# Kernel optimization log

Measured on AMD Instinct MI355X. Metric: run time of the kernel, lower is better.

## Reference

```python
import jax, jax.numpy as jnp
import numpy as np

N_CLASS = 20
N_SIGMA = 2
H = W = 512
B = 4
N_INST = 32
W_INST, W_VAR, W_SEED = 1.0, 10.0, 1.0
FG_WEIGHT = 10.0


def _xym():
    # channel 0: x along width, channel 1: y along height (matches torch buffer)
    xm = jnp.broadcast_to(jnp.linspace(0.0, 1.0, W)[None, :], (H, W))
    ym = jnp.broadcast_to(jnp.linspace(0.0, 1.0, H)[:, None], (H, W))
    return jnp.stack([xm, ym], axis=0)  # [2, H, W]


def lovasz_hinge_flat(logits, gt, valid):
    # logits, gt (0/1 float), valid (bool), all flat [P]; ignored pixels excluded
    P = logits.shape[0]
    vf = valid.astype(logits.dtype)
    signs = 2.0 * gt - 1.0
    # push ignored pixels to the end of the descending sort; relu(-1e9)=0 kills them
    errors = jnp.where(valid, 1.0 - logits * signs, -1e9)
    errors_sorted, perm = jax.lax.top_k(errors, P)  # descending
    gt_sorted = jnp.take(gt * vf, perm)
    v_sorted = jnp.take(vf, perm)
    gts = jnp.sum(gt * vf)
    inter = gts - jnp.cumsum(gt_sorted)
    union = gts + jnp.cumsum((1.0 - gt_sorted) * v_sorted)
    jac = 1.0 - inter / jnp.maximum(union, 1e-9)
    jac = jnp.concatenate([jac[:1], jac[1:] - jac[:-1]])
    return jnp.sum(jax.nn.relu(errors_sorted) * jac)


def _per_image(pred_b, inst_b, lab_b, xym, fg_w, n_inst):
    spatial_emb = jnp.tanh(pred_b[:2]) + xym            # [2,H,W]
    sigma = pred_b[2:2 + N_SIGMA]                       # [n_sigma,H,W]
    seed = jax.nn.sigmoid(pred_b[2 + N_SIGMA:2 + N_SIGMA + N_CLASS])  # [C,H,W]
    inst = inst_b[0]
    lab = lab_b[0]
    valid = (lab != 255)

    # background seed loss: sum over classes of seed^2 on pixels not of that class
    cls_ids = jnp.arange(N_CLASS)
    bg = (lab[None] != (cls_ids + 1)[:, None, None]) & valid[None]
    seed_bg = jnp.sum(jnp.square(seed) * bg)

    def per_inst(iid):
        m = (inst == iid)
        mf = m.astype(pred_b.dtype)
        cnt = jnp.maximum(jnp.sum(mf), 1.0)
        # to_center=True: center is mean coordinate of instance pixels
        center = jnp.sum(xym * mf[None], axis=(1, 2)) / cnt          # [2]
        s_mean = jnp.sum(sigma * mf[None], axis=(1, 2)) / cnt        # [n_sigma]
        var_l = jnp.sum(jnp.square(sigma - jax.lax.stop_gradient(s_mean)[:, None, None]) * mf[None]) / (N_SIGMA * cnt)
        s = jnp.exp(s_mean * 10.0)
        dist = jnp.exp(-jnp.sum(jnp.square(spatial_emb - center[:, None, None]) * s[:, None, None], axis=0))  # [H,W]
        inst_l = lovasz_hinge_flat((dist * 2.0 - 1.0).reshape(-1), mf.reshape(-1), valid.reshape(-1))
        cls = jnp.max(lab * m) - 1  # instance class (0-indexed)
        seed_c = jnp.take(seed, cls, axis=0)
        seed_fg = jnp.take(fg_w, cls) * jnp.sum(jnp.square(seed_c - jax.lax.stop_gradient(dist)) * mf)
        return inst_l, var_l, seed_fg

    inst_ls, var_ls, seed_fgs = jax.vmap(per_inst)(jnp.arange(1, n_inst + 1))
    instance_loss = jnp.sum(inst_ls) / n_inst
    var_loss = jnp.sum(var_ls) / n_inst
    seed_loss = (seed_bg + jnp.sum(seed_fgs)) / (H * W)
    return W_INST * instance_loss + W_VAR * var_loss + W_SEED * seed_loss


def setup_inputs() -> dict:
    key = jax.random.key(0)
    k1, k2 = jax.random.split(key)
    prediction = jax.random.normal(k1, (B, 2 + N_SIGMA + N_CLASS, H, W), dtype=jnp.float32)
    instances = jax.random.randint(k2, (B, 1, H, W), 0, N_INST + 1).astype(jnp.int32)
    # each instance id has a consistent class, as the torch instance_to_cls dict assumes
    labels = jnp.where(instances > 0, ((instances - 1) % N_CLASS) + 1, 0).astype(jnp.int32)
    return {"prediction": prediction, "instances": instances, "labels": labels, "n_instances": N_INST}


def reference(prediction, instances, labels, n_instances):
    xym = _xym()
    fg_w = jnp.full((N_CLASS,), FG_WEIGHT, dtype=prediction.dtype)
    per = jax.vmap(lambda p, i, l: _per_image(p, i, l, xym, fg_w, n_instances))(prediction, instances, labels)
    return jnp.mean(per) + jnp.sum(prediction) * 0.0
```

## Files before the change

### kernel.cpp

```cpp
#include <hip/hip_runtime.h>
#include <hip/hip_fp16.h>
#include <math.h>

#define HH 512
#define WW 512
#define BB 4
#define NCLS 20
#define NINST 32
#define NPIX (HH*WW)
#define NCH 24
#define NBIN 128
#define NCHUNK3 256
#define CPX3 1024
#define K3T 512
#define HSTR 33

#define OFF_PARTA  ((size_t)0)
#define OFF_PSEED  (OFF_PARTA + 1024*256*4)
#define OFF_STATS  (OFF_PSEED + 1024*8)
#define OFF_SEEDBG (OFF_STATS + 8*128*4)
#define OFF_VALID  (OFF_SEEDBG + 4*4)
#define OFF_INSTL  (OFF_VALID + 4*4)
#define OFF_SFG    (OFF_INSTL + 128*4)
#define OFF_CNT    (OFF_SFG + 1024*4)
#define OFF_REC    ((OFF_CNT + 4 + 255) & ~(size_t)255)
#define OFF_HIST   (OFF_REC + (size_t)BB*NPIX*8)

__device__ __forceinline__ float fast_rcp(float x) { return __builtin_amdgcn_rcpf(x); }
__device__ __forceinline__ float fast_sigmoid(float z) { return fast_rcp(1.0f + __expf(-z)); }
__device__ __forceinline__ float fast_tanh(float x) {
  return 1.0f - 2.0f * fast_rcp(__expf(2.0f * x) + 1.0f);
}

__global__ __launch_bounds__(256) void k1_stats(
    const float* __restrict__ pred, const int* __restrict__ inst,
    const int* __restrict__ lab,
    float* __restrict__ partA, float2* __restrict__ partSeed,
    uint2* __restrict__ rec)
{
  __shared__ unsigned s_st[4][NINST][9];
  __shared__ float s_seed, s_valid;
  int t = threadIdx.x;
  int w = t >> 6;
  for (int i = t; i < 4*NINST*9; i += 256) ((unsigned*)s_st)[i] = 0u;
  if (t == 0) { s_seed = 0.f; s_valid = 0.f; }
  __syncthreads();

  int b = blockIdx.x >> 8;
  int blk = blockIdx.x & 255;
  const float* pb = pred + (size_t)b*NCH*NPIX;

  int p = blk*1024 + t*4;
  float4 e0v = *(const float4*)(pb + p);
  float4 e1v = *(const float4*)(pb + NPIX + p);
  float4 g0v = *(const float4*)(pb + 2*NPIX + p);
  float4 g1v = *(const float4*)(pb + 3*NPIX + p);
  int4 idv = *(const int4*)(inst + (size_t)b*NPIX + p);
  int4 lbv = *(const int4*)(lab + (size_t)b*NPIX + p);

  float vloc = 0.f;
  #pragma unroll
  for (int u = 0; u < 4; ++u) {
    int px = p + u;
    int x = px & (WW-1);
    int y = px >> 9;
    float xm = x * (1.0f/(WW-1));
    float ym = y * (1.0f/(HH-1));
    float g0 = (&g0v.x)[u];
    float g1 = (&g1v.x)[u];
    int id = (&idv.x)[u];
    int lb = (&lbv.x)[u];
    if (lb != 255) vloc += 1.0f;
    if (id >= 1) {
      int j = id - 1;
      unsigned* row = s_st[w][j];
      atomicAdd(&row[0], 1u | ((lb != 255) ? 0x10000u : 0u));
      atomicAdd((float*)&row[1], xm);
      atomicAdd((float*)&row[2], ym);
      atomicAdd((float*)&row[3], g0);
      atomicAdd((float*)&row[4], g1);
      atomicAdd((float*)&row[5], g0*g0);
      atomicAdd((float*)&row[6], g1*g1);
    }
  }

  float seedloc = 0.f;
  float so[4] = {0.f,0.f,0.f,0.f};
  float Sv[4] = {0.f,0.f,0.f,0.f};
  for (int c = 0; c < NCLS; ++c) {
    float4 sv = *(const float4*)(pb + (size_t)(4+c)*NPIX + p);
    #pragma unroll
    for (int u = 0; u < 4; ++u) {
      float sg = fast_sigmoid((&sv.x)[u]);
      Sv[u] += sg*sg;
      if (c + 1 == (&lbv.x)[u]) so[u] = sg;
    }
  }
  #pragma unroll
  for (int u = 0; u < 4; ++u)
    if ((&lbv.x)[u] != 255) seedloc += Sv[u] - so[u]*so[u];

  {
    uint2 r4[4];
    #pragma unroll
    for (int u = 0; u < 4; ++u) {
      int px = p + u;
      int x = px & (WW-1);
      int y = px >> 9;
      float ex = fast_tanh((&e0v.x)[u]) + x * (1.0f/(WW-1));
      float ey = fast_tanh((&e1v.x)[u]) + y * (1.0f/(HH-1));
      __half2 h = __floats2half2_rn(ex, ey);
      unsigned valid = ((&lbv.x)[u] != 255) ? 1u : 0u;
      unsigned meta = (unsigned)(&idv.x)[u] | (valid << 7);
      r4[u].x = *reinterpret_cast<unsigned*>(&h);
      r4[u].y = (unsigned)(unsigned char)(so[u]*255.f + 0.5f) | (meta << 8);
    }
    uint4* dst = (uint4*)(rec + (size_t)b*NPIX + p);
    dst[0] = make_uint4(r4[0].x, r4[0].y, r4[1].x, r4[1].y);
    dst[1] = make_uint4(r4[2].x, r4[2].y, r4[3].x, r4[3].y);
  }
  for (int o = 32; o; o >>= 1) {
    seedloc += __shfl_down(seedloc, o);
    vloc    += __shfl_down(vloc, o);
  }
  if ((t & 63) == 0) { atomicAdd(&s_seed, seedloc); atomicAdd(&s_valid, vloc); }
  __syncthreads();

  {
    int j = t & 31, f = t >> 5;
    float v;
    if (f == 0) {
      unsigned s = (s_st[0][j][0] & 0xFFFFu) + (s_st[1][j][0] & 0xFFFFu)
                 + (s_st[2][j][0] & 0xFFFFu) + (s_st[3][j][0] & 0xFFFFu);
      v = (float)s;
    } else if (f == 7) {
      unsigned s = (s_st[0][j][0] >> 16) + (s_st[1][j][0] >> 16)
                 + (s_st[2][j][0] >> 16) + (s_st[3][j][0] >> 16);
      v = (float)s;
    } else {
      v = __uint_as_float(s_st[0][j][f]) + __uint_as_float(s_st[1][j][f])
        + __uint_as_float(s_st[2][j][f]) + __uint_as_float(s_st[3][j][f]);
    }
    partA[(blockIdx.x << 8) + t] = v;
  }
  if (t == 0) partSeed[blockIdx.x] = make_float2(s_seed, s_valid);
}

__global__ __launch_bounds__(256) void k2a_reduce(
    const float* __restrict__ partA, const float2* __restrict__ partSeed,
    float* __restrict__ stats, float* __restrict__ seedbg,
    float* __restrict__ validT, unsigned* __restrict__ counter)
{
  int bid = blockIdx.x;
  int t = threadIdx.x;
  if (bid < 32) {
    __shared__ float red[256];
    int b = bid >> 3, f = bid & 7;
    int j = t & 31, grp = t >> 5;
    float s = 0.f;
    #pragma unroll 8
    for (int k = 0; k < 32; ++k)
      s += partA[((b*256 + grp*32 + k) << 8) + (f << 5) + j];
    red[t] = s; __syncthreads();
    for (int st = 128; st >= 32; st >>= 1) {
      if (t < st) red[t] += red[t + st];
      __syncthreads();
    }
    if (t < 32) stats[f*128 + b*32 + t] = red[t];
  } else {
    if (t == 0) counter[0] = 0u;
    int img = t >> 6, slot = t & 63;
    float s = 0.f, v = 0.f;
    #pragma unroll
    for (int k = 0; k < 4; ++k) {
      float2 ps = partSeed[img*256 + slot*4 + k];
      s += ps.x; v += ps.y;
    }
    for (int o = 32; o; o >>= 1) {
      s += __shfl_down(s, o);
      v += __shfl_down(v, o);
    }
    if (slot == 0) { seedbg[img] = s; validT[img] = v; }
  }
}

__global__ __launch_bounds__(K3T) void k3_hist(
    const uint2* __restrict__ rec, const float* __restrict__ stats,
    unsigned* __restrict__ hist, float* __restrict__ sfg)
{
  __shared__ unsigned hc[NBIN*HSTR];
  __shared__ float sder[NINST][4];
  __shared__ float s_fg[8];
  int t = threadIdx.x;
  int bid = blockIdx.x;
  int b = bid >> 8;
  int chunk = bid & 255;
  for (int i = t; i < NBIN*HSTR; i += K3T) hc[i] = 0u;
  if (t < NINST) {
    int pr = b*NINST + t;
    float cnt = fmaxf(stats[0*128+pr], 1.0f);
    float rc = fast_rcp(cnt);
    sder[t][0] = stats[1*128+pr] * rc;
    sder[t][1] = stats[2*128+pr] * rc;
    sder[t][2] = -1.442695041f * __expf(10.f * stats[3*128+pr] * rc);
    sder[t][3] = -1.442695041f * __expf(10.f * stats[4*128+pr] * rc);
  }
  __syncthreads();

  int w = t >> 6, lane = t & 63;
  int j = lane & 31, jp1 = j + 1;
  float cx = sder[j][0], cy = sder[j][1];
  float s0 = sder[j][2], s1 = sder[j][3];
  const uint2* rb = rec + (size_t)b*NPIX + chunk*CPX3 + w*128;

  float fg = 0.f;
  #pragma unroll 4
  for (int r = 0; r < 64; ++r) {
    uint2 rv = rb[r*2 + (lane >> 5)];
    __half2 h;
    *reinterpret_cast<unsigned*>(&h) = rv.x;
    float2 e = __half22float2(h);
    unsigned hi = rv.y;
    float dx = e.x - cx, dy = e.y - cy;
    float dist = exp2f(dx*dx*s0 + dy*dy*s1);
    bool own = ((int)((hi >> 8) & 0x3F) == jp1);
    if (own) { float d = (float)(hi & 0xFFu)*(1.0f/255.f) - dist; fg += d*d; }
    if (hi & 0x8000u) {
      float f = own ? (1.0f - dist) : dist;
      unsigned bin = min((unsigned)(f * (float)NBIN), NBIN-1u);
      if (bin) atomicAdd(&hc[bin*HSTR + j], own ? 0x10001u : 1u);
    }
  }
  for (int o = 32; o; o >>= 1) fg += __shfl_down(fg, o);
  if (lane == 0) s_fg[w] = fg;
  __syncthreads();
  if (t == 0) {
    float s = 0.f;
    #pragma unroll
    for (int i = 0; i < 8; ++i) s += s_fg[i];
    sfg[bid] = 10.0f * s;
  }
  unsigned* out = hist + (size_t)(b*NCHUNK3 + chunk) * (NINST*NBIN);
  #pragma unroll
  for (int k = 0; k < NINST*NBIN/K3T; ++k) {
    int idx = k*K3T + t;
    out[idx] = hc[(idx & 127)*HSTR + (idx >> 7)];
  }
}

__global__ __launch_bounds__(512) void k45_scan_final(
    const unsigned* __restrict__ hist, const float* __restrict__ stats,
    const float* __restrict__ validT, const float* __restrict__ seedbg,
    const float* __restrict__ sfg, float* __restrict__ instl,
    unsigned* __restrict__ counter, float* __restrict__ out)
{
  __shared__ unsigned s_c[4][NBIN], s_p[4][NBIN];
  __shared__ unsigned rc[NBIN], rp[NBIN];
  __shared__ float redf[512];
  __shared__ int lastflag;
  int t = threadIdx.x;
  int pair = blockIdx.x;
  int b = pair >> 5, j = pair & 31;
  int grp = t >> 7, bin = t & 127;
  const unsigned* bp = hist + ((size_t)b*NCHUNK3*NINST + j)*NBIN + bin;
  unsigned c = 0, p = 0;
  #pragma unroll 8
  for (int ch = grp*64; ch < grp*64 + 64; ++ch) {
    unsigned v = bp[(size_t)ch * (NINST*NBIN)];
    c += v & 0xFFFFu; p += v >> 16;
  }
  s_c[grp][bin] = c; s_p[grp][bin] = p;
  __syncthreads();
  if (t < NBIN) {
    unsigned cc = s_c[0][t] + s_c[1][t] + s_c[2][t] + s_c[3][t];
    unsigned pp = s_p[0][t] + s_p[1][t] + s_p[2][t] + s_p[3][t];
    s_c[0][t] = cc; s_p[0][t] = pp;
    rc[t] = t ? cc : 0u; rp[t] = t ? pp : 0u;
  }
  __syncthreads();
  for (int st = 64; st; st >>= 1) {
    if (t < st) { rc[t] += rc[t+st]; rp[t] += rp[t+st]; }
    __syncthreads();
  }
  float G = stats[7*128+pair];
  if (t == 0) {
    s_c[0][0] = (unsigned)validT[b] - rc[0];
    s_p[0][0] = (unsigned)G - rp[0];
  }
  __syncthreads();

  if (t < 64) {
    int lane = t;
    unsigned carryN = 0, carryP = 0;
    float Jprev = 0.f, L = 0.f;
    for (int c8 = 0; c8 < NBIN/64; ++c8) {
      int k = NBIN - 1 - c8*64 - lane;
      unsigned n = s_c[0][k], pp0 = s_p[0][k];
      for (int off = 1; off < 64; off <<= 1) {
        unsigned nn = __shfl_up(n, off);
        unsigned pq = __shfl_up(pp0, off);
        if (lane >= off) { n += nn; pp0 += pq; }
      }
      float fN = (float)(carryN + n);
      float fP = (float)(carryP + pp0);
      float uni = G + fN - fP;
      float J = 1.0f - (G - fP) / fmaxf(uni, 1e-9f);
      float Jp = __shfl_up(J, 1);
      if (lane == 0) Jp = Jprev;
      float v = (k + 0.5f) * (2.0f/NBIN);
      L += v * (J - Jp);
      carryN += __shfl(n, 63);
      carryP += __shfl(pp0, 63);
      Jprev  = __shfl(J, 63);
    }
    for (int o = 32; o; o >>= 1) L += __shfl_down(L, o);
    if (lane == 0) instl[pair] = L;
  }
  __threadfence();
  __syncthreads();
  if (t == 0) {
    unsigned old = atomicAdd(counter, 1u);
    lastflag = (old == 127u) ? 1 : 0;
  }
  __syncthreads();
  if (!lastflag) return;

  float acc = (sfg[t] + sfg[t + 512]) * (1.0f/NPIX);
  if (t < 4) acc += seedbg[t] * (1.0f/NPIX);
  if (t < 128) {
    float cntA = stats[0*128+t];
    float cnt = fmaxf(cntA, 1.0f);
    float s0 = stats[3*128+t], s1 = stats[4*128+t];
    float q0 = stats[5*128+t], q1 = stats[6*128+t];
    float sm0 = s0/cnt, sm1 = s1/cnt;
    float varnum = q0 - 2.f*sm0*s0 + cntA*sm0*sm0
                 + q1 - 2.f*sm1*s1 + cntA*sm1*sm1;
    float varl = varnum / (2.0f * cnt);
    float il = atomicAdd(&instl[t], 0.0f);
    acc += (il + 10.0f*varl) * (1.0f/NINST);
  }
  redf[t] = acc; __syncthreads();
  for (int st = 256; st; st >>= 1) {
    if (t < st) redf[t] += redf[t+st];
    __syncthreads();
  }
  if (t == 0) out[0] = redf[0] * (1.0f/BB);
}

extern "C" void kernel_launch(void* const* d_in, const int* in_sizes, int n_in,
                              void* d_out, int out_size, void* d_ws, size_t ws_size,
                              hipStream_t stream)
{
  const float* pred = (const float*)d_in[0];
  const int* inst = (const int*)d_in[1];
  const int* lab  = (const int*)d_in[2];
  char* ws = (char*)d_ws;
  float* partA = (float*)(ws + OFF_PARTA);
  float2* partSeed = (float2*)(ws + OFF_PSEED);
  float* stats = (float*)(ws + OFF_STATS);
  float* seedbg = (float*)(ws + OFF_SEEDBG);
  float* validT = (float*)(ws + OFF_VALID);
  float* instl = (float*)(ws + OFF_INSTL);
  float* sfg = (float*)(ws + OFF_SFG);
  unsigned* counter = (unsigned*)(ws + OFF_CNT);
  uint2* rec = (uint2*)(ws + OFF_REC);
  unsigned* hist = (unsigned*)(ws + OFF_HIST);

  hipLaunchKernelGGL(k1_stats, dim3(1024), dim3(256), 0, stream,
                     pred, inst, lab, partA, partSeed, rec);
  hipLaunchKernelGGL(k2a_reduce, dim3(33), dim3(256), 0, stream,
                     partA, partSeed, stats, seedbg, validT, counter);
  hipLaunchKernelGGL(k3_hist, dim3(BB*NCHUNK3), dim3(K3T), 0, stream,
                     rec, stats, hist, sfg);
  hipLaunchKernelGGL(k45_scan_final, dim3(128), dim3(512), 0, stream,
                     hist, stats, validT, seedbg, sfg, instl, counter, (float*)d_out);
}
```

Before: 103.8 us.

## Split seed and geometry passes into separate kernels, replace last-block counter with final kernel

The fused stats kernel is split in two. One kernel computes the sigmoid seed sums and writes a packed per-pixel byte of the own-class seed. The other does the instance geometry atomics and packs records using that byte. The last-block atomic counter pattern in the scan kernel is replaced by a separate single-block final reduction kernel. The split is meant to cut register and shared-memory pressure in each kernel, at the cost of two extra launches and an extra 1 MB workspace round trip.

```diff
diff --git a/kernel.cpp b/kernel.cpp
--- a/kernel.cpp
+++ b/kernel.cpp
@@ -22,8 +22,8 @@
 #define OFF_VALID  (OFF_SEEDBG + 4*4)
 #define OFF_INSTL  (OFF_VALID + 4*4)
 #define OFF_SFG    (OFF_INSTL + 128*4)
-#define OFF_CNT    (OFF_SFG + 1024*4)
-#define OFF_REC    ((OFF_CNT + 4 + 255) & ~(size_t)255)
+#define OFF_SGOWN  ((OFF_SFG + 1024*4 + 255) & ~(size_t)255)
+#define OFF_REC    (OFF_SGOWN + (size_t)BB*NPIX)
 #define OFF_HIST   (OFF_REC + (size_t)BB*NPIX*8)
 
 __device__ __forceinline__ float fast_rcp(float x) { return __builtin_amdgcn_rcpf(x); }
@@ -32,33 +32,72 @@
   return 1.0f - 2.0f * fast_rcp(__expf(2.0f * x) + 1.0f);
 }
 
-__global__ __launch_bounds__(256) void k1_stats(
+__global__ __launch_bounds__(256) void k1b_seed(
+    const float* __restrict__ pred, const int* __restrict__ lab,
+    float2* __restrict__ partSeed, unsigned char* __restrict__ sgown)
+{
+  __shared__ float s_seed, s_valid;
+  int t = threadIdx.x;
+  if (t == 0) { s_seed = 0.f; s_valid = 0.f; }
+  __syncthreads();
+
+  int b = blockIdx.x >> 8;
+  int p = (blockIdx.x & 255) * 1024 + t * 4;
+  const float* pb = pred + (size_t)b*NCH*NPIX;
+  int4 lbv = *(const int4*)(lab + (size_t)b*NPIX + p);
+
+  float so[4] = {0.f,0.f,0.f,0.f};
+  float Sv[4] = {0.f,0.f,0.f,0.f};
+  #pragma unroll 5
+  for (int c = 0; c < NCLS; ++c) {
+    float4 sv = *(const float4*)(pb + (size_t)(4+c)*NPIX + p);
+    #pragma unroll
+    for (int u = 0; u < 4; ++u) {
+      float sg = fast_sigmoid((&sv.x)[u]);
+      Sv[u] += sg*sg;
+      if (c + 1 == (&lbv.x)[u]) so[u] = sg;
+    }
+  }
+  float seedloc = 0.f, vloc = 0.f;
+  unsigned pk = 0;
+  #pragma unroll
+  for (int u = 0; u < 4; ++u) {
+    if ((&lbv.x)[u] != 255) { seedloc += Sv[u] - so[u]*so[u]; vloc += 1.0f; }
+    pk |= ((unsigned)(unsigned char)(so[u]*255.f + 0.5f)) << (8*u);
+  }
+  *(unsigned*)(sgown + (size_t)b*NPIX + p) = pk;
+
+  for (int o = 32; o; o >>= 1) {
+    seedloc += __shfl_down(seedloc, o);
+    vloc    += __shfl_down(vloc, o);
+  }
+  if ((t & 63) == 0) { atomicAdd(&s_seed, seedloc); atomicAdd(&s_valid, vloc); }
+  __syncthreads();
+  if (t == 0) partSeed[blockIdx.x] = make_float2(s_seed, s_valid);
+}
+
+__global__ __launch_bounds__(256) void k1a_geom(
     const float* __restrict__ pred, const int* __restrict__ inst,
-    const int* __restrict__ lab,
-    float* __restrict__ partA, float2* __restrict__ partSeed,
-    uint2* __restrict__ rec)
+    const int* __restrict__ lab, const unsigned char* __restrict__ sgown,
+    float* __restrict__ partA, uint2* __restrict__ rec)
 {
   __shared__ unsigned s_st[4][NINST][9];
-  __shared__ float s_seed, s_valid;
   int t = threadIdx.x;
   int w = t >> 6;
   for (int i = t; i < 4*NINST*9; i += 256) ((unsigned*)s_st)[i] = 0u;
-  if (t == 0) { s_seed = 0.f; s_valid = 0.f; }
   __syncthreads();
 
   int b = blockIdx.x >> 8;
-  int blk = blockIdx.x & 255;
+  int p = (blockIdx.x & 255) * 1024 + t * 4;
   const float* pb = pred + (size_t)b*NCH*NPIX;
-
-  int p = blk*1024 + t*4;
   float4 e0v = *(const float4*)(pb + p);
   float4 e1v = *(const float4*)(pb + NPIX + p);
   float4 g0v = *(const float4*)(pb + 2*NPIX + p);
   float4 g1v = *(const float4*)(pb + 3*NPIX + p);
   int4 idv = *(const int4*)(inst + (size_t)b*NPIX + p);
   int4 lbv = *(const int4*)(lab + (size_t)b*NPIX + p);
-
-  float vloc = 0.f;
+  unsigned sg4 = *(const unsigned*)(sgown + (size_t)b*NPIX + p);
+
   #pragma unroll
   for (int u = 0; u < 4; ++u) {
     int px = p + u;
@@ -70,7 +109,6 @@
     float g1 = (&g1v.x)[u];
     int id = (&idv.x)[u];
     int lb = (&lbv.x)[u];
-    if (lb != 255) vloc += 1.0f;
     if (id >= 1) {
       int j = id - 1;
       unsigned* row = s_st[w][j];
@@ -83,22 +121,6 @@
       atomicAdd((float*)&row[6], g1*g1);
     }
   }
-
-  float seedloc = 0.f;
-  float so[4] = {0.f,0.f,0.f,0.f};
-  float Sv[4] = {0.f,0.f,0.f,0.f};
-  for (int c = 0; c < NCLS; ++c) {
-    float4 sv = *(const float4*)(pb + (size_t)(4+c)*NPIX + p);
-    #pragma unroll
-    for (int u = 0; u < 4; ++u) {
-      float sg = fast_sigmoid((&sv.x)[u]);
-      Sv[u] += sg*sg;
-      if (c + 1 == (&lbv.x)[u]) so[u] = sg;
-    }
-  }
-  #pragma unroll
-  for (int u = 0; u < 4; ++u)
-    if ((&lbv.x)[u] != 255) seedloc += Sv[u] - so[u]*so[u];
 
   {
     uint2 r4[4];
@@ -113,19 +135,13 @@
       unsigned valid = ((&lbv.x)[u] != 255) ? 1u : 0u;
       unsigned meta = (unsigned)(&idv.x)[u] | (valid << 7);
       r4[u].x = *reinterpret_cast<unsigned*>(&h);
-      r4[u].y = (unsigned)(unsigned char)(so[u]*255.f + 0.5f) | (meta << 8);
+      r4[u].y = ((sg4 >> (8*u)) & 0xFFu) | (meta << 8);
     }
     uint4* dst = (uint4*)(rec + (size_t)b*NPIX + p);
     dst[0] = make_uint4(r4[0].x, r4[0].y, r4[1].x, r4[1].y);
     dst[1] = make_uint4(r4[2].x, r4[2].y, r4[3].x, r4[3].y);
   }
-  for (int o = 32; o; o >>= 1) {
-    seedloc += __shfl_down(seedloc, o);
-    vloc    += __shfl_down(vloc, o);
-  }
-  if ((t & 63) == 0) { atomicAdd(&s_seed, seedloc); atomicAdd(&s_valid, vloc); }
-  __syncthreads();
-
+  __syncthreads();
   {
     int j = t & 31, f = t >> 5;
     float v;
@@ -143,13 +159,12 @@
     }
     partA[(blockIdx.x << 8) + t] = v;
   }
-  if (t == 0) partSeed[blockIdx.x] = make_float2(s_seed, s_valid);
 }
 
 __global__ __launch_bounds__(256) void k2a_reduce(
     const float* __restrict__ partA, const float2* __restrict__ partSeed,
     float* __restrict__ stats, float* __restrict__ seedbg,
-    float* __restrict__ validT, unsigned* __restrict__ counter)
+    float* __restrict__ validT)
 {
   int bid = blockIdx.x;
   int t = threadIdx.x;
@@ -168,7 +183,6 @@
     }
     if (t < 32) stats[f*128 + b*32 + t] = red[t];
   } else {
-    if (t == 0) counter[0] = 0u;
     int img = t >> 6, slot = t & 63;
     float s = 0.f, v = 0.f;
     #pragma unroll
@@ -248,16 +262,12 @@
   }
 }
 
-__global__ __launch_bounds__(512) void k45_scan_final(
+__global__ __launch_bounds__(512) void k4_scan(
     const unsigned* __restrict__ hist, const float* __restrict__ stats,
-    const float* __restrict__ validT, const float* __restrict__ seedbg,
-    const float* __restrict__ sfg, float* __restrict__ instl,
-    unsigned* __restrict__ counter, float* __restrict__ out)
+    const float* __restrict__ validT, float* __restrict__ instl)
 {
   __shared__ unsigned s_c[4][NBIN], s_p[4][NBIN];
   __shared__ unsigned rc[NBIN], rp[NBIN];
-  __shared__ float redf[512];
-  __shared__ int lastflag;
   int t = threadIdx.x;
   int pair = blockIdx.x;
   int b = pair >> 5, j = pair & 31;
@@ -316,15 +326,15 @@
     for (int o = 32; o; o >>= 1) L += __shfl_down(L, o);
     if (lane == 0) instl[pair] = L;
   }
-  __threadfence();
-  __syncthreads();
-  if (t == 0) {
-    unsigned old = atomicAdd(counter, 1u);
-    lastflag = (old == 127u) ? 1 : 0;
-  }
-  __syncthreads();
-  if (!lastflag) return;
-
+}
+
+__global__ __launch_bounds__(512) void k5_final(
+    const float* __restrict__ instl, const float* __restrict__ stats,
+    const float* __restrict__ seedbg, const float* __restrict__ sfg,
+    float* __restrict__ out)
+{
+  __shared__ float red[512];
+  int t = threadIdx.x;
   float acc = (sfg[t] + sfg[t + 512]) * (1.0f/NPIX);
   if (t < 4) acc += seedbg[t] * (1.0f/NPIX);
   if (t < 128) {
@@ -336,15 +346,14 @@
     float varnum = q0 - 2.f*sm0*s0 + cntA*sm0*sm0
                  + q1 - 2.f*sm1*s1 + cntA*sm1*sm1;
     float varl = varnum / (2.0f * cnt);
-    float il = atomicAdd(&instl[t], 0.0f);
-    acc += (il + 10.0f*varl) * (1.0f/NINST);
-  }
-  redf[t] = acc; __syncthreads();
+    acc += (instl[t] + 10.0f*varl) * (1.0f/NINST);
+  }
+  red[t] = acc; __syncthreads();
   for (int st = 256; st; st >>= 1) {
-    if (t < st) redf[t] += redf[t+st];
+    if (t < st) red[t] += red[t+st];
     __syncthreads();
   }
-  if (t == 0) out[0] = redf[0] * (1.0f/BB);
+  if (t == 0) out[0] = red[0] * (1.0f/BB);
 }
 
 extern "C" void kernel_launch(void* const* d_in, const int* in_sizes, int n_in,
@@ -362,16 +371,20 @@
   float* validT = (float*)(ws + OFF_VALID);
   float* instl = (float*)(ws + OFF_INSTL);
   float* sfg = (float*)(ws + OFF_SFG);
-  unsigned* counter = (unsigned*)(ws + OFF_CNT);
+  unsigned char* sgown = (unsigned char*)(ws + OFF_SGOWN);
   uint2* rec = (uint2*)(ws + OFF_REC);
   unsigned* hist = (unsigned*)(ws + OFF_HIST);
 
-  hipLaunchKernelGGL(k1_stats, dim3(1024), dim3(256), 0, stream,
-                     pred, inst, lab, partA, partSeed, rec);
+  hipLaunchKernelGGL(k1b_seed, dim3(1024), dim3(256), 0, stream,
+                     pred, lab, partSeed, sgown);
+  hipLaunchKernelGGL(k1a_geom, dim3(1024), dim3(256), 0, stream,
+                     pred, inst, lab, sgown, partA, rec);
   hipLaunchKernelGGL(k2a_reduce, dim3(33), dim3(256), 0, stream,
-                     partA, partSeed, stats, seedbg, validT, counter);
+                     partA, partSeed, stats, seedbg, validT);
   hipLaunchKernelGGL(k3_hist, dim3(BB*NCHUNK3), dim3(K3T), 0, stream,
                      rec, stats, hist, sfg);
-  hipLaunchKernelGGL(k45_scan_final, dim3(128), dim3(512), 0, stream,
-                     hist, stats, validT, seedbg, sfg, instl, counter, (float*)d_out);
-}
+  hipLaunchKernelGGL(k4_scan, dim3(128), dim3(512), 0, stream,
+                     hist, stats, validT, instl);
+  hipLaunchKernelGGL(k5_final, dim3(1), dim3(512), 0, stream,
+                     instl, stats, seedbg, sfg, (float*)d_out);
+}
```

Result: no change. 101.9 us (-1.8%).
